# Optimization experiments

Measured on AMD Instinct MI355X. Metric: run time of the kernel, lower is better.

The kernel has to match this reference:

```python
import jax, jax.numpy as jnp
import numpy as np

N_QUBITS = 10
DEPTH = 6


def _ry(theta):
    # RY(theta) = [[cos(t/2), -sin(t/2)], [sin(t/2), cos(t/2)]]
    c = jnp.cos(theta / 2)
    s = jnp.sin(theta / 2)
    return jnp.stack([jnp.stack([c, -s]), jnp.stack([s, c])]).astype(jnp.complex64)


def _rot(phi, theta, omega):
    # PennyLane Rot(phi, theta, omega) = RZ(omega) RY(theta) RZ(phi)
    c = jnp.cos(theta / 2)
    s = jnp.sin(theta / 2)
    ep = jnp.exp(-0.5j * (phi + omega).astype(jnp.complex64))
    em = jnp.exp(-0.5j * (phi - omega).astype(jnp.complex64))
    return jnp.stack([
        jnp.stack([ep * c, -jnp.conj(em) * s]),
        jnp.stack([em * s, jnp.conj(ep) * c]),
    ])


def _apply_1q(psi, U, w):
    # psi: (2,)*n statevector; apply 2x2 unitary U on qubit axis w
    psi = jnp.tensordot(U, psi, axes=([1], [w]))
    return jnp.moveaxis(psi, 0, w)


def _apply_cnot(psi, c, t):
    # flip target axis t on the control=1 slice of axis c
    psi = jnp.moveaxis(psi, (c, t), (0, 1))
    psi = jnp.concatenate([psi[:1], psi[1:, ::-1]], axis=0)
    return jnp.moveaxis(psi, (0, 1), (c, t))


def _circuit(angles, weights):
    """RY encoding + StronglyEntanglingLayers + PauliZ expvals. angles: (n,), weights: (depth, n, 3)."""
    n = N_QUBITS
    psi = jnp.zeros((2,) * n, jnp.complex64).at[(0,) * n].set(1.0)
    for i in range(n):
        psi = _apply_1q(psi, _ry(angles[i]), i)
    for l in range(DEPTH):
        for i in range(n):
            psi = _apply_1q(psi, _rot(weights[l, i, 0], weights[l, i, 1], weights[l, i, 2]), i)
        r = (l % (n - 1)) + 1  # default StronglyEntanglingLayers range schedule
        for i in range(n):
            psi = _apply_cnot(psi, i, (i + r) % n)
    p = psi.real ** 2 + psi.imag ** 2  # probabilities, shape (2,)*n
    exps = []
    for i in range(n):
        pm = jnp.moveaxis(p, i, 0).reshape(2, -1).sum(axis=1)
        exps.append(pm[0] - pm[1])  # <Z_i>
    return jnp.stack(exps)


def setup_inputs() -> dict:
    key = jax.random.key(0)
    ks = jax.random.split(key, 5)
    B, F, C = 8192, 1024, 10
    x = jax.random.normal(ks[0], (B, F), jnp.float32)
    W_proj = jax.random.normal(ks[1], (N_QUBITS, F), jnp.float32) / np.sqrt(F).astype(np.float32)
    weights = 0.01 * jax.random.normal(ks[2], (DEPTH, N_QUBITS, 3), jnp.float32)
    W_out = jax.random.normal(ks[3], (C, N_QUBITS), jnp.float32) / np.sqrt(N_QUBITS).astype(np.float32)
    b_out = 0.01 * jax.random.normal(ks[4], (C,), jnp.float32)
    return {"x": x, "W_proj": W_proj, "weights": weights, "W_out": W_out, "b_out": b_out}


def reference(x, W_proj, weights, W_out, b_out):
    # classical projection + angle encoding
    angles = jnp.tanh(x @ W_proj.T) * jnp.float32(np.pi / 2)  # (B, n_qubits)
    # batched exact statevector simulation of the VQC
    q = jax.vmap(_circuit, in_axes=(0, None))(angles, weights)  # (B, n_qubits)
    return q @ W_out.T + b_out  # (B, num_classes)
```

## Files before the change

### kernel.cpp

```cpp
#include <hip/hip_runtime.h>
#include <math.h>
#include <stdint.h>

#define NQ 10
#define DEPTH 6

typedef _Float16 f16x8 __attribute__((ext_vector_type(8)));
typedef float f32x4 __attribute__((ext_vector_type(4)));

typedef __attribute__((address_space(3))) unsigned int lds_u32;
typedef const __attribute__((address_space(1))) unsigned int glb_u32;

__device__ __forceinline__ void async_load16(const unsigned short* g, unsigned short* l) {
    __builtin_amdgcn_global_load_lds((glb_u32*)g, (lds_u32*)l, 16, 0, 0);
}

__global__ void prep_gates_kernel(const float* __restrict__ weights,
                                  float* __restrict__ gmat) {
    int idx = blockIdx.x * blockDim.x + threadIdx.x;
    if (idx >= DEPTH * NQ) return;
    float phi   = weights[idx * 3 + 0];
    float theta = weights[idx * 3 + 1];
    float omega = weights[idx * 3 + 2];
    float c = cosf(0.5f * theta), s = sinf(0.5f * theta);
    float ap = -0.5f * (phi + omega);
    float am = -0.5f * (phi - omega);
    float epr = cosf(ap), epi = sinf(ap);
    float emr = cosf(am), emi = sinf(am);
    float* g = gmat + idx * 8;
    g[0] =  epr * c;  g[1] =  epi * c;
    g[2] = -emr * s;  g[3] =  emi * s;
    g[4] =  emr * s;  g[5] =  emi * s;
    g[6] =  epr * c;  g[7] = -epi * c;
}

__device__ __forceinline__ void apply_1q_local(
    float (&ar)[16], float (&ai)[16], int q,
    float u00r, float u00i, float u01r, float u01i,
    float u10r, float u10i, float u11r, float u11i) {
#pragma unroll
    for (int j = 0; j < 16; ++j) {
        if ((j >> q) & 1) continue;
        int j1 = j | (1 << q);
        float a0r = ar[j],  a0i = ai[j];
        float a1r = ar[j1], a1i = ai[j1];
        ar[j]  = u00r*a0r - u00i*a0i + u01r*a1r - u01i*a1i;
        ai[j]  = u00r*a0i + u00i*a0r + u01r*a1i + u01i*a1r;
        ar[j1] = u10r*a0r - u10i*a0i + u11r*a1r - u11i*a1i;
        ai[j1] = u10r*a0i + u10i*a0r + u11r*a1i + u11i*a1r;
    }
}

__device__ __forceinline__ void apply_1q_lane(
    float (&ar)[16], float (&ai)[16], int q, int lane,
    float u00r, float u00i, float u01r, float u01i,
    float u10r, float u10i, float u11r, float u11i) {
    int  m  = 1 << (q - 4);
    bool hi = (lane >> (q - 4)) & 1;
    float car = hi ? u11r : u00r, cai = hi ? u11i : u00i;
    float cbr = hi ? u10r : u01r, cbi = hi ? u10i : u01i;
    float pr[16], pi[16];
#pragma unroll
    for (int j = 0; j < 16; ++j) pr[j] = __shfl_xor(ar[j], m, 64);
#pragma unroll
    for (int j = 0; j < 16; ++j) pi[j] = __shfl_xor(ai[j], m, 64);
#pragma unroll
    for (int j = 0; j < 16; ++j) {
        float mr = ar[j], mi = ai[j];
        ar[j] = car*mr - cai*mi + cbr*pr[j] - cbi*pi[j];
        ai[j] = car*mi + cai*mr + cbr*pi[j] + cbi*pr[j];
    }
}

__device__ __forceinline__ void cnot_gate(
    float (&ar)[16], float (&ai)[16], int c, int t, int lane) {
    if (c < 4 && t < 4) {
#pragma unroll
        for (int j = 0; j < 16; ++j) {
            if (((j >> c) & 1) && !((j >> t) & 1)) {
                int j1 = j | (1 << t);
                float tr = ar[j]; ar[j] = ar[j1]; ar[j1] = tr;
                float ti = ai[j]; ai[j] = ai[j1]; ai[j1] = ti;
            }
        }
    } else if (c < 4) {
        int m = 1 << (t - 4);
        float pr[16], pi[16];
#pragma unroll
        for (int j = 0; j < 16; ++j)
            if ((j >> c) & 1) pr[j] = __shfl_xor(ar[j], m, 64);
#pragma unroll
        for (int j = 0; j < 16; ++j)
            if ((j >> c) & 1) pi[j] = __shfl_xor(ai[j], m, 64);
#pragma unroll
        for (int j = 0; j < 16; ++j)
            if ((j >> c) & 1) { ar[j] = pr[j]; ai[j] = pi[j]; }
    } else if (t < 4) {
        bool cb = (lane >> (c - 4)) & 1;
#pragma unroll
        for (int j = 0; j < 16; ++j) {
            if (!((j >> t) & 1)) {
                int j1 = j | (1 << t);
                float lr = ar[j], li = ai[j], hr = ar[j1], hi2 = ai[j1];
                ar[j]  = cb ? hr : lr;  ai[j]  = cb ? hi2 : li;
                ar[j1] = cb ? lr : hr;  ai[j1] = cb ? li : hi2;
            }
        }
    } else {
        int  m  = 1 << (t - 4);
        bool cb = (lane >> (c - 4)) & 1;
        float pr[16], pi[16];
#pragma unroll
        for (int j = 0; j < 16; ++j) pr[j] = __shfl_xor(ar[j], m, 64);
#pragma unroll
        for (int j = 0; j < 16; ++j) pi[j] = __shfl_xor(ai[j], m, 64);
#pragma unroll
        for (int j = 0; j < 16; ++j) {
            ar[j] = cb ? pr[j] : ar[j];
            ai[j] = cb ? pi[j] : ai[j];
        }
    }
}

template <int R>
__device__ __forceinline__ void cnot_ring(float (&ar)[16], float (&ai)[16], int lane) {
#pragma unroll
    for (int i = 0; i < NQ; ++i) cnot_gate(ar, ai, i, (i + R) % NQ, lane);
}

__device__ __forceinline__ void run_circuit(float (&ar)[16], float (&ai)[16],
                                            const float* __restrict__ gmat, int lane) {
    for (int l = 0; l < DEPTH; ++l) {
        const float* gl = gmat + l * (NQ * 8);
#pragma unroll
        for (int i = 0; i < NQ; ++i) {
            const float* g = gl + i * 8;
            float u00r = g[0], u00i = g[1], u01r = g[2], u01i = g[3];
            float u10r = g[4], u10i = g[5], u11r = g[6], u11i = g[7];
            if (i < 4)
                apply_1q_local(ar, ai, i, u00r,u00i,u01r,u01i,u10r,u10i,u11r,u11i);
            else
                apply_1q_lane(ar, ai, i, lane, u00r,u00i,u01r,u01i,u10r,u10i,u11r,u11i);
        }
        switch (l) {
            case 0: cnot_ring<1>(ar, ai, lane); break;
            case 1: cnot_ring<2>(ar, ai, lane); break;
            case 2: cnot_ring<3>(ar, ai, lane); break;
            case 3: cnot_ring<4>(ar, ai, lane); break;
            case 4: cnot_ring<5>(ar, ai, lane); break;
            default: cnot_ring<6>(ar, ai, lane); break;
        }
    }
}

__device__ __forceinline__ float wave_sum(float v) {
#pragma unroll
    for (int m = 1; m < 64; m <<= 1) v += __shfl_xor(v, m, 64);
    return v;
}

__device__ __forceinline__ void basis_sim_body(
    const float* __restrict__ gmat, _Float16* __restrict__ Bp, int h, int lane) {
    float ar[16], ai[16];
#pragma unroll
    for (int j = 0; j < 16; ++j) {
        ar[j] = (lane == (h >> 4) && j == (h & 15)) ? 1.f : 0.f;
        ai[j] = 0.f;
    }
    run_circuit(ar, ai, gmat, lane);

    unsigned int buf[16];
#pragma unroll
    for (int j = 0; j < 16; ++j) {
        unsigned short r16 = __builtin_bit_cast(unsigned short, (_Float16)ar[j]);
        unsigned short i16 = __builtin_bit_cast(unsigned short, (_Float16)ai[j]);
        buf[j] = (unsigned int)r16 | ((unsigned int)i16 << 16);
    }
    uint4* dst = (uint4*)(Bp + (size_t)h * 2048 + 32 * lane);
#pragma unroll
    for (int k = 0; k < 4; ++k) {
        uint4 v; v.x = buf[k*4+0]; v.y = buf[k*4+1]; v.z = buf[k*4+2]; v.w = buf[k*4+3];
        dst[k] = v;
    }
}

__device__ __forceinline__ void proj_v_body(
    const float* __restrict__ x, const float* __restrict__ Wproj,
    _Float16* __restrict__ V, int b, int lane) {
    const float* xb = x + (size_t)b * 1024;
    float acc[NQ];
#pragma unroll
    for (int q = 0; q < NQ; ++q) acc[q] = 0.f;
#pragma unroll
    for (int k = 0; k < 16; ++k) {
        float xv = xb[k * 64 + lane];
#pragma unroll
        for (int q = 0; q < NQ; ++q)
            acc[q] = fmaf(xv, Wproj[q * 1024 + k * 64 + lane], acc[q]);
    }
#pragma unroll
    for (int q = 0; q < NQ; ++q) acc[q] = wave_sum(acc[q]);

    float cq[NQ], sq[NQ];
#pragma unroll
    for (int q = 0; q < NQ; ++q) {
        float ang = tanhf(acc[q]) * 1.57079632679489662f;
        cq[q] = cosf(0.5f * ang);
        sq[q] = sinf(0.5f * ang);
    }
    float laneprod = 1.f;
#pragma unroll
    for (int q = 4; q < NQ; ++q)
        laneprod *= ((lane >> (q - 4)) & 1) ? sq[q] : cq[q];

    unsigned int buf[8];
#pragma unroll
    for (int jj = 0; jj < 8; ++jj) {
        unsigned short h2[2];
#pragma unroll
        for (int c = 0; c < 2; ++c) {
            int j = jj * 2 + c;
            float p = laneprod;
#pragma unroll
            for (int q = 0; q < 4; ++q) p *= ((j >> q) & 1) ? sq[q] : cq[q];
            h2[c] = __builtin_bit_cast(unsigned short, (_Float16)p);
        }
        buf[jj] = (unsigned int)h2[0] | ((unsigned int)h2[1] << 16);
    }
    uint4* dst = (uint4*)(V + (size_t)b * 1024 + 16 * lane);
    uint4 v0; v0.x = buf[0]; v0.y = buf[1]; v0.z = buf[2]; v0.w = buf[3];
    uint4 v1; v1.x = buf[4]; v1.y = buf[5]; v1.z = buf[6]; v1.w = buf[7];
    dst[0] = v0; dst[1] = v1;
}

__global__ __launch_bounds__(256) void basis_proj_kernel(
    const float* __restrict__ gmat, _Float16* __restrict__ Bp,
    const float* __restrict__ x, const float* __restrict__ Wproj,
    _Float16* __restrict__ V, int B) {
    int lane = threadIdx.x & 63;
    int wid  = threadIdx.x >> 6;
    if (blockIdx.x < 256) {
        int h = blockIdx.x * 4 + wid;
        basis_sim_body(gmat, Bp, h, lane);
    } else {
        int b = (blockIdx.x - 256) * 4 + wid;
        if (b < B) proj_v_body(x, Wproj, V, b, lane);
    }
}

__global__ __launch_bounds__(256) void transpose_kernel(
    const unsigned short* __restrict__ src, unsigned short* __restrict__ dst) {
    __shared__ unsigned short tile[64][65];
    int bx = blockIdx.x;
    int by = blockIdx.y;
    int tx = threadIdx.x & 63;
    int ty = threadIdx.x >> 6;
#pragma unroll
    for (int i = 0; i < 16; ++i) {
        int r = ty + i * 4;
        tile[r][tx] = src[(size_t)(by*64 + r) * 2048 + bx*64 + tx];
    }
    __syncthreads();
#pragma unroll
    for (int i = 0; i < 16; ++i) {
        int r = ty + i * 4;
        dst[(size_t)(bx*64 + r) * 1024 + by*64 + tx] = tile[tx][r];
    }
}

__global__ __launch_bounds__(256) void gemm_fused_kernel(
    const unsigned short* __restrict__ A,
    const unsigned short* __restrict__ Bt,
    float* __restrict__ Zpart) {
    __shared__ unsigned short As[128 * 64];
    __shared__ unsigned short Bs[128 * 64];
    int tid  = threadIdx.x;
    int lane = tid & 63;
    int w    = tid >> 6;
    int m0   = blockIdx.x * 128;
    int n0   = blockIdx.y * 128;
    int mh   = (w >> 1) * 64, nh = (w & 1) * 64;
    int quad = lane >> 4;
    int lrow = lane & 15;

    int srow  = (lane >> 3);
    int schnk = (lane & 7) ^ srow;

    f32x4 acc[4][4];
#pragma unroll
    for (int mi = 0; mi < 4; ++mi)
#pragma unroll
        for (int ni = 0; ni < 4; ++ni)
            acc[mi][ni] = (f32x4){0.f, 0.f, 0.f, 0.f};

    for (int kt = 0; kt < 16; ++kt) {
        if (kt) __syncthreads();
#pragma unroll
        for (int r = 0; r < 4; ++r) {
            int s   = w * 4 + r;
            int row = s * 8 + srow;
            async_load16(A  + (size_t)(m0 + row) * 1024 + kt * 64 + schnk * 8,
                         As + s * 512);
            async_load16(Bt + (size_t)(n0 + row) * 1024 + kt * 64 + schnk * 8,
                         Bs + s * 512);
        }
        asm volatile("s_waitcnt vmcnt(0)" ::: "memory");
        __syncthreads();
#pragma unroll
        for (int kk = 0; kk < 2; ++kk) {
            f16x8 af[4], bf[4];
#pragma unroll
            for (int i = 0; i < 4; ++i) {
                int cxa = (kk * 4 + quad) ^ (lrow & 7);
                af[i] = *(const f16x8*)(As + (mh + i * 16 + lrow) * 64 + cxa * 8);
                bf[i] = *(const f16x8*)(Bs + (nh + i * 16 + lrow) * 64 + cxa * 8);
            }
#pragma unroll
            for (int mi = 0; mi < 4; ++mi)
#pragma unroll
                for (int ni = 0; ni < 4; ++ni)
                    acc[mi][ni] = __builtin_amdgcn_mfma_f32_16x16x32_f16(
                        af[mi], bf[ni], acc[mi][ni], 0, 0, 0);
        }
    }

    __syncthreads();
    float* Zs = (float*)As;
#pragma unroll
    for (int mi = 0; mi < 4; ++mi) {
#pragma unroll
        for (int r = 0; r < 4; ++r) {
            float p0 = acc[mi][0][r] * acc[mi][0][r];
            float p1 = acc[mi][1][r] * acc[mi][1][r];
            float p2 = acc[mi][2][r] * acc[mi][2][r];
            float p3 = acc[mi][3][r] * acc[mi][3][r];
            float t0 = (p0 + p1) + (p2 + p3);
            float t3 = (p0 - p1) + (p2 - p3);
            float t4 = (p0 + p1) - (p2 + p3);
            t0 += __shfl_xor(t0, 1, 64);
            t3 += __shfl_xor(t3, 1, 64);
            t4 += __shfl_xor(t4, 1, 64);
            float u2 = __shfl_xor(t0, 2, 64);
            float ap = t0 + u2;
            float am = (lane & 2) ? u2 - t0 : t0 - u2;
            t3 += __shfl_xor(t3, 2, 64);
            t4 += __shfl_xor(t4, 2, 64);
            float u4  = __shfl_xor(ap, 4, 64);
            float bpp = ap + u4;
            float bpm = (lane & 4) ? u4 - ap : ap - u4;
            float bmp = am + __shfl_xor(am, 4, 64);
            t3 += __shfl_xor(t3, 4, 64);
            t4 += __shfl_xor(t4, 4, 64);
            float u8 = __shfl_xor(bpp, 8, 64);
            float T  = bpp + u8;
            float Z2 = (lane & 8) ? u8 - bpp : bpp - u8;
            float Z1 = bpm + __shfl_xor(bpm, 8, 64);
            float Z0 = bmp + __shfl_xor(bmp, 8, 64);
            t3 += __shfl_xor(t3, 8, 64);
            t4 += __shfl_xor(t4, 8, 64);
            if (lrow == 0) {
                int row = mh + mi * 16 + quad * 4 + r;
                float* z = Zs + ((size_t)(w & 1) * 128 + row) * 8;
                z[0] = T;  z[1] = Z0; z[2] = Z1; z[3] = Z2;
                z[4] = t3; z[5] = t4;
            }
        }
    }
    __syncthreads();
    {
        int row  = tid >> 1, part = tid & 1;
        const float* za = Zs + (size_t)row * 8;
        const float* zb = Zs + (size_t)(128 + row) * 8;
        float o[4];
        if (part == 0) {
            o[0] = za[0] + zb[0];
            o[1] = za[1] + zb[1];
            o[2] = za[2] + zb[2];
            o[3] = za[3] + zb[3];
        } else {
            o[0] = za[4] + zb[4];
            o[1] = za[5] + zb[5];
            o[2] = za[0] - zb[0];
            o[3] = 0.f;
        }
        float4 v = {o[0], o[1], o[2], o[3]};
        *(float4*)(Zpart + ((size_t)(m0 + row) * 16 + blockIdx.y) * 8 + part * 4) = v;
    }
}

__global__ __launch_bounds__(256) void combine_head_kernel(
    const float* __restrict__ Zpart, const float* __restrict__ Wout,
    const float* __restrict__ bout, float* __restrict__ out, int B) {
    int lane = threadIdx.x & 63;
    int wid  = threadIdx.x >> 6;
    int b    = blockIdx.x * 4 + wid;
    if (b >= B) return;

    float z[8];
    if (lane < 16) {
        const float4* p = (const float4*)(Zpart + ((size_t)b * 16 + lane) * 8);
        float4 a = p[0], c = p[1];
        z[0]=a.x; z[1]=a.y; z[2]=a.z; z[3]=a.w; z[4]=c.x; z[5]=c.y; z[6]=c.z; z[7]=c.w;
    } else {
#pragma unroll
        for (int i = 0; i < 8; ++i) z[i] = 0.f;
    }
    float Zq[NQ];
#pragma unroll
    for (int q = 0; q < 6; ++q) {
        float v = z[q + 1];
        v += __shfl_xor(v, 1, 64);
        v += __shfl_xor(v, 2, 64);
        v += __shfl_xor(v, 4, 64);
        v += __shfl_xor(v, 8, 64);
        Zq[q] = v;
    }
    {
        float T = z[0];
        float u1 = __shfl_xor(T, 1, 64);
        float P  = T + u1;
        float M  = (lane & 1) ? u1 - T : T - u1;
        float u2 = __shfl_xor(P, 2, 64);
        float PP = P + u2;
        float PM = (lane & 2) ? u2 - P : P - u2;
        float MP = M + __shfl_xor(M, 2, 64);
        float u4  = __shfl_xor(PP, 4, 64);
        float PPP = PP + u4;
        float PPM = (lane & 4) ? u4 - PP : PP - u4;
        float PMP = PM + __shfl_xor(PM, 4, 64);
        float MPP = MP + __shfl_xor(MP, 4, 64);
        float u8 = __shfl_xor(PPP, 8, 64);
        Zq[9] = (lane & 8) ? u8 - PPP : PPP - u8;
        Zq[8] = PPM + __shfl_xor(PPM, 8, 64);
        Zq[7] = PMP + __shfl_xor(PMP, 8, 64);
        Zq[6] = MPP + __shfl_xor(MPP, 8, 64);
    }
    if (lane < NQ) {
        float o = bout[lane];
#pragma unroll
        for (int q = 0; q < NQ; ++q) o = fmaf(Zq[q], Wout[lane * NQ + q], o);
        out[(size_t)b * NQ + lane] = o;
    }
}

__global__ __launch_bounds__(256) void vqc_kernel(
    const float* __restrict__ x, const float* __restrict__ Wproj,
    const float* __restrict__ gmat, const float* __restrict__ Wout,
    const float* __restrict__ bout, float* __restrict__ out, int B) {
    int lane = threadIdx.x & 63;
    int wid  = threadIdx.x >> 6;
    int b    = blockIdx.x * 4 + wid;
    if (b >= B) return;

    const float* xb = x + (size_t)b * 1024;
    float acc[NQ];
#pragma unroll
    for (int q = 0; q < NQ; ++q) acc[q] = 0.f;
#pragma unroll
    for (int k = 0; k < 16; ++k) {
        float xv = xb[k * 64 + lane];
#pragma unroll
        for (int q = 0; q < NQ; ++q)
            acc[q] = fmaf(xv, Wproj[q * 1024 + k * 64 + lane], acc[q]);
    }
#pragma unroll
    for (int q = 0; q < NQ; ++q) acc[q] = wave_sum(acc[q]);

    float cq[NQ], sq[NQ];
#pragma unroll
    for (int q = 0; q < NQ; ++q) {
        float ang = tanhf(acc[q]) * 1.57079632679489662f;
        cq[q] = cosf(0.5f * ang);
        sq[q] = sinf(0.5f * ang);
    }
    float laneprod = 1.f;
#pragma unroll
    for (int q = 4; q < NQ; ++q)
        laneprod *= ((lane >> (q - 4)) & 1) ? sq[q] : cq[q];
    float ar[16], ai[16];
#pragma unroll
    for (int j = 0; j < 16; ++j) {
        float p = laneprod;
#pragma unroll
        for (int q = 0; q < 4; ++q) p *= ((j >> q) & 1) ? sq[q] : cq[q];
        ar[j] = p; ai[j] = 0.f;
    }
    run_circuit(ar, ai, gmat, lane);

    float T = 0.f, S[4] = {0.f, 0.f, 0.f, 0.f};
#pragma unroll
    for (int j = 0; j < 16; ++j) {
        float p = ar[j] * ar[j] + ai[j] * ai[j];
        T += p;
#pragma unroll
        for (int q = 0; q < 4; ++q) S[q] += ((j >> q) & 1) ? -p : p;
    }
    float Zq[NQ];
#pragma unroll
    for (int q = 0; q < 4; ++q) Zq[q] = S[q];
#pragma unroll
    for (int q = 4; q < NQ; ++q) Zq[q] = ((lane >> (q - 4)) & 1) ? -T : T;
#pragma unroll
    for (int q = 0; q < NQ; ++q) Zq[q] = wave_sum(Zq[q]);
    if (lane < NQ) {
        float o = bout[lane];
#pragma unroll
        for (int q = 0; q < NQ; ++q) o = fmaf(Zq[q], Wout[lane * NQ + q], o);
        out[(size_t)b * NQ + lane] = o;
    }
}

extern "C" void kernel_launch(void* const* d_in, const int* in_sizes, int n_in,
                              void* d_out, int out_size, void* d_ws, size_t ws_size,
                              hipStream_t stream) {
    const float* x       = (const float*)d_in[0];
    const float* Wproj   = (const float*)d_in[1];
    const float* weights = (const float*)d_in[2];
    const float* Wout    = (const float*)d_in[3];
    const float* bout    = (const float*)d_in[4];
    float* out = (float*)d_out;
    int B = in_sizes[0] / 1024;

    char* ws = (char*)d_ws;
    size_t off_Bp = 4096;
    size_t off_Bt = off_Bp + (size_t)1024 * 2048 * 2;
    size_t off_V  = off_Bt + (size_t)2048 * 1024 * 2;
    size_t off_Z  = off_V  + (size_t)B * 1024 * 2;
    size_t need   = off_Z  + (size_t)B * 16 * 8 * 4;

    float* gmat = (float*)ws;
    prep_gates_kernel<<<1, 64, 0, stream>>>(weights, gmat);

    if (ws_size >= need && (B % 128) == 0) {
        _Float16* Bp = (_Float16*)(ws + off_Bp);
        _Float16* Bt = (_Float16*)(ws + off_Bt);
        _Float16* V  = (_Float16*)(ws + off_V);
        float*  Zprt = (float*)(ws + off_Z);

        basis_proj_kernel<<<256 + B / 4, 256, 0, stream>>>(gmat, Bp, x, Wproj, V, B);
        transpose_kernel<<<dim3(32, 16), 256, 0, stream>>>(
            (const unsigned short*)Bp, (unsigned short*)Bt);
        gemm_fused_kernel<<<dim3(B / 128, 16), 256, 0, stream>>>(
            (const unsigned short*)V, (const unsigned short*)Bt, Zprt);
        combine_head_kernel<<<B / 4, 256, 0, stream>>>(Zprt, Wout, bout, out, B);
    } else {
        vqc_kernel<<<(B + 3) / 4, 256, 0, stream>>>(x, Wproj, gmat, Wout, bout, out, B);
    }
}
```

Baseline: 172.1 us.

## Fuse gate prep and transpose into basis simulation kernel, vectorize projection loads

Gate matrices are now computed per block into shared memory inside the basis kernel, so the separate prep launch goes away. Each basis block stages its four simulated columns in LDS and writes them straight into the transposed layout, which removes the standalone transpose kernel and the intermediate buffer. The projection loop now uses float4 loads for x and W_proj. The price is redundant gate computation in every block and narrow 8-byte strided stores into Bt, which coalesce poorly.

```diff
diff --git a/kernel.cpp b/kernel.cpp
--- a/kernel.cpp
+++ b/kernel.cpp
@@ -15,10 +15,8 @@
     __builtin_amdgcn_global_load_lds((glb_u32*)g, (lds_u32*)l, 16, 0, 0);
 }
 
-__global__ void prep_gates_kernel(const float* __restrict__ weights,
-                                  float* __restrict__ gmat) {
-    int idx = blockIdx.x * blockDim.x + threadIdx.x;
-    if (idx >= DEPTH * NQ) return;
+__device__ __forceinline__ void compute_gate(const float* __restrict__ weights,
+                                             int idx, float* __restrict__ g) {
     float phi   = weights[idx * 3 + 0];
     float theta = weights[idx * 3 + 1];
     float omega = weights[idx * 3 + 2];
@@ -27,11 +25,17 @@
     float am = -0.5f * (phi - omega);
     float epr = cosf(ap), epi = sinf(ap);
     float emr = cosf(am), emi = sinf(am);
-    float* g = gmat + idx * 8;
     g[0] =  epr * c;  g[1] =  epi * c;
     g[2] = -emr * s;  g[3] =  emi * s;
     g[4] =  emr * s;  g[5] =  emi * s;
     g[6] =  epr * c;  g[7] = -epi * c;
+}
+
+__global__ void prep_gates_kernel(const float* __restrict__ weights,
+                                  float* __restrict__ gmat) {
+    int idx = blockIdx.x * blockDim.x + threadIdx.x;
+    if (idx >= DEPTH * NQ) return;
+    compute_gate(weights, idx, gmat + idx * 8);
 }
 
 __device__ __forceinline__ void apply_1q_local(
@@ -159,44 +163,25 @@
     return v;
 }
 
-__device__ __forceinline__ void basis_sim_body(
-    const float* __restrict__ gmat, _Float16* __restrict__ Bp, int h, int lane) {
-    float ar[16], ai[16];
-#pragma unroll
-    for (int j = 0; j < 16; ++j) {
-        ar[j] = (lane == (h >> 4) && j == (h & 15)) ? 1.f : 0.f;
-        ai[j] = 0.f;
-    }
-    run_circuit(ar, ai, gmat, lane);
-
-    unsigned int buf[16];
-#pragma unroll
-    for (int j = 0; j < 16; ++j) {
-        unsigned short r16 = __builtin_bit_cast(unsigned short, (_Float16)ar[j]);
-        unsigned short i16 = __builtin_bit_cast(unsigned short, (_Float16)ai[j]);
-        buf[j] = (unsigned int)r16 | ((unsigned int)i16 << 16);
-    }
-    uint4* dst = (uint4*)(Bp + (size_t)h * 2048 + 32 * lane);
-#pragma unroll
-    for (int k = 0; k < 4; ++k) {
-        uint4 v; v.x = buf[k*4+0]; v.y = buf[k*4+1]; v.z = buf[k*4+2]; v.w = buf[k*4+3];
-        dst[k] = v;
-    }
-}
-
 __device__ __forceinline__ void proj_v_body(
     const float* __restrict__ x, const float* __restrict__ Wproj,
     _Float16* __restrict__ V, int b, int lane) {
-    const float* xb = x + (size_t)b * 1024;
+    const float4* xb4 = (const float4*)(x + (size_t)b * 1024);
+    const float4* W4  = (const float4*)Wproj;
     float acc[NQ];
 #pragma unroll
     for (int q = 0; q < NQ; ++q) acc[q] = 0.f;
 #pragma unroll
-    for (int k = 0; k < 16; ++k) {
-        float xv = xb[k * 64 + lane];
-#pragma unroll
-        for (int q = 0; q < NQ; ++q)
-            acc[q] = fmaf(xv, Wproj[q * 1024 + k * 64 + lane], acc[q]);
+    for (int k4 = 0; k4 < 4; ++k4) {
+        float4 xv = xb4[k4 * 64 + lane];
+#pragma unroll
+        for (int q = 0; q < NQ; ++q) {
+            float4 wv = W4[q * 256 + k4 * 64 + lane];
+            acc[q] = fmaf(xv.x, wv.x, acc[q]);
+            acc[q] = fmaf(xv.y, wv.y, acc[q]);
+            acc[q] = fmaf(xv.z, wv.z, acc[q]);
+            acc[q] = fmaf(xv.w, wv.w, acc[q]);
+        }
     }
 #pragma unroll
     for (int q = 0; q < NQ; ++q) acc[q] = wave_sum(acc[q]);
@@ -234,55 +219,67 @@
 }
 
 __global__ __launch_bounds__(256) void basis_proj_kernel(
-    const float* __restrict__ gmat, _Float16* __restrict__ Bp,
+    const float* __restrict__ weights, _Float16* __restrict__ Bt,
     const float* __restrict__ x, const float* __restrict__ Wproj,
     _Float16* __restrict__ V, int B) {
-    int lane = threadIdx.x & 63;
-    int wid  = threadIdx.x >> 6;
-    if (blockIdx.x < 256) {
-        int h = blockIdx.x * 4 + wid;
-        basis_sim_body(gmat, Bp, h, lane);
-    } else {
-        int b = (blockIdx.x - 256) * 4 + wid;
-        if (b < B) proj_v_body(x, Wproj, V, b, lane);
-    }
-}
-
-__global__ __launch_bounds__(256) void transpose_kernel(
-    const unsigned short* __restrict__ src, unsigned short* __restrict__ dst) {
-    __shared__ unsigned short tile[64][65];
-    int bx = blockIdx.x;
-    int by = blockIdx.y;
-    int tx = threadIdx.x & 63;
-    int ty = threadIdx.x >> 6;
-#pragma unroll
-    for (int i = 0; i < 16; ++i) {
-        int r = ty + i * 4;
-        tile[r][tx] = src[(size_t)(by*64 + r) * 2048 + bx*64 + tx];
-    }
-    __syncthreads();
-#pragma unroll
-    for (int i = 0; i < 16; ++i) {
-        int r = ty + i * 4;
-        dst[(size_t)(bx*64 + r) * 1024 + by*64 + tx] = tile[tx][r];
-    }
-}
-
-__global__ __launch_bounds__(256) void gemm_fused_kernel(
-    const unsigned short* __restrict__ A,
-    const unsigned short* __restrict__ Bt,
-    float* __restrict__ Zpart) {
-    __shared__ unsigned short As[128 * 64];
-    __shared__ unsigned short Bs[128 * 64];
+    __shared__ float gmat_s[DEPTH * NQ * 8];
+    __shared__ unsigned short colbuf[4][2048];
     int tid  = threadIdx.x;
     int lane = tid & 63;
     int w    = tid >> 6;
-    int m0   = blockIdx.x * 128;
-    int n0   = blockIdx.y * 128;
+
+    if (blockIdx.x < 256) {
+        int j = blockIdx.x;
+        if (tid < DEPTH * NQ) compute_gate(weights, tid, gmat_s + tid * 8);
+        __syncthreads();
+
+        int h = j * 4 + w;
+        float ar[16], ai[16];
+#pragma unroll
+        for (int jj = 0; jj < 16; ++jj) {
+            ar[jj] = (lane == (h >> 4) && jj == (h & 15)) ? 1.f : 0.f;
+            ai[jj] = 0.f;
+        }
+        run_circuit(ar, ai, gmat_s, lane);
+
+        unsigned int buf[16];
+#pragma unroll
+        for (int jj = 0; jj < 16; ++jj) {
+            unsigned short r16 = __builtin_bit_cast(unsigned short, (_Float16)ar[jj]);
+            unsigned short i16 = __builtin_bit_cast(unsigned short, (_Float16)ai[jj]);
+            buf[jj] = (unsigned int)r16 | ((unsigned int)i16 << 16);
+        }
+        uint4* cdst = (uint4*)&colbuf[w][32 * lane];
+#pragma unroll
+        for (int k = 0; k < 4; ++k) {
+            uint4 v; v.x = buf[k*4+0]; v.y = buf[k*4+1]; v.z = buf[k*4+2]; v.w = buf[k*4+3];
+            cdst[k] = v;
+        }
+        __syncthreads();
+        unsigned short* btp = (unsigned short*)Bt + (size_t)j * 4;
+#pragma unroll
+        for (int i = 0; i < 8; ++i) {
+            int n = i * 256 + tid;
+            unsigned int lo = (unsigned int)colbuf[0][n] | ((unsigned int)colbuf[1][n] << 16);
+            unsigned int hi = (unsigned int)colbuf[2][n] | ((unsigned int)colbuf[3][n] << 16);
+            uint2 v; v.x = lo; v.y = hi;
+            *(uint2*)(btp + (size_t)n * 1024) = v;
+        }
+    } else {
+        int b = (blockIdx.x - 256) * 4 + w;
+        if (b < B) proj_v_body(x, Wproj, V, b, lane);
+    }
+}
+
+__device__ __forceinline__ void gemm_tile_body(
+    unsigned short* As, unsigned short* Bs,
+    const unsigned short* __restrict__ A, const unsigned short* __restrict__ Bt,
+    float* __restrict__ Zpart, int m0, int n0, int nb, int tid) {
+    int lane = tid & 63;
+    int w    = tid >> 6;
     int mh   = (w >> 1) * 64, nh = (w & 1) * 64;
     int quad = lane >> 4;
     int lrow = lane & 15;
-
     int srow  = (lane >> 3);
     int schnk = (lane & 7) ^ srow;
 
@@ -384,18 +381,22 @@
             o[3] = 0.f;
         }
         float4 v = {o[0], o[1], o[2], o[3]};
-        *(float4*)(Zpart + ((size_t)(m0 + row) * 16 + blockIdx.y) * 8 + part * 4) = v;
-    }
-}
-
-__global__ __launch_bounds__(256) void combine_head_kernel(
+        *(float4*)(Zpart + ((size_t)(m0 + row) * 16 + nb) * 8 + part * 4) = v;
+    }
+}
+
+__global__ __launch_bounds__(256) void gemm_fused_kernel(
+    const unsigned short* __restrict__ A, const unsigned short* __restrict__ Bt,
+    float* __restrict__ Zpart) {
+    __shared__ unsigned short As[128 * 64];
+    __shared__ unsigned short Bs[128 * 64];
+    gemm_tile_body(As, Bs, A, Bt, Zpart,
+                   blockIdx.x * 128, blockIdx.y * 128, blockIdx.y, threadIdx.x);
+}
+
+__device__ __forceinline__ void combine_head_body(
     const float* __restrict__ Zpart, const float* __restrict__ Wout,
-    const float* __restrict__ bout, float* __restrict__ out, int B) {
-    int lane = threadIdx.x & 63;
-    int wid  = threadIdx.x >> 6;
-    int b    = blockIdx.x * 4 + wid;
-    if (b >= B) return;
-
+    const float* __restrict__ bout, float* __restrict__ out, int b, int lane) {
     float z[8];
     if (lane < 16) {
         const float4* p = (const float4*)(Zpart + ((size_t)b * 16 + lane) * 8);
@@ -443,6 +444,16 @@
     }
 }
 
+__global__ __launch_bounds__(256) void combine_head_kernel(
+    const float* __restrict__ Zpart, const float* __restrict__ Wout,
+    const float* __restrict__ bout, float* __restrict__ out, int B) {
+    int lane = threadIdx.x & 63;
+    int wid  = threadIdx.x >> 6;
+    int b    = blockIdx.x * 4 + wid;
+    if (b >= B) return;
+    combine_head_body(Zpart, Wout, bout, out, b, lane);
+}
+
 __global__ __launch_bounds__(256) void vqc_kernel(
     const float* __restrict__ x, const float* __restrict__ Wproj,
     const float* __restrict__ gmat, const float* __restrict__ Wout,
@@ -522,28 +533,23 @@
     int B = in_sizes[0] / 1024;
 
     char* ws = (char*)d_ws;
-    size_t off_Bp = 4096;
-    size_t off_Bt = off_Bp + (size_t)1024 * 2048 * 2;
+    size_t off_Bt = 4096;
     size_t off_V  = off_Bt + (size_t)2048 * 1024 * 2;
     size_t off_Z  = off_V  + (size_t)B * 1024 * 2;
     size_t need   = off_Z  + (size_t)B * 16 * 8 * 4;
 
-    float* gmat = (float*)ws;
-    prep_gates_kernel<<<1, 64, 0, stream>>>(weights, gmat);
-
     if (ws_size >= need && (B % 128) == 0) {
-        _Float16* Bp = (_Float16*)(ws + off_Bp);
         _Float16* Bt = (_Float16*)(ws + off_Bt);
         _Float16* V  = (_Float16*)(ws + off_V);
         float*  Zprt = (float*)(ws + off_Z);
 
-        basis_proj_kernel<<<256 + B / 4, 256, 0, stream>>>(gmat, Bp, x, Wproj, V, B);
-        transpose_kernel<<<dim3(32, 16), 256, 0, stream>>>(
-            (const unsigned short*)Bp, (unsigned short*)Bt);
+        basis_proj_kernel<<<256 + B / 4, 256, 0, stream>>>(weights, Bt, x, Wproj, V, B);
         gemm_fused_kernel<<<dim3(B / 128, 16), 256, 0, stream>>>(
             (const unsigned short*)V, (const unsigned short*)Bt, Zprt);
         combine_head_kernel<<<B / 4, 256, 0, stream>>>(Zprt, Wout, bout, out, B);
     } else {
+        float* gmat = (float*)ws;
+        prep_gates_kernel<<<1, 64, 0, stream>>>(weights, gmat);
         vqc_kernel<<<(B + 3) / 4, 256, 0, stream>>>(x, Wproj, gmat, Wout, bout, out, B);
     }
 }
```

New measurement: 170.2 us. About the same (-1.1%).
